# Kernel tuning notes

Measured on AMD Instinct MI355X. Metric: run time of the kernel, lower is better.

## Reference

```python
import jax, jax.numpy as jnp
import numpy as np

N = 100000          # batch_size == number of tree nodes
F = 512             # feature_size
C = 512             # number_of_features_to_detect
WINDOW_DEPTH = 3    # depth_of_sliding_window


def _build_tree(rng, n):
    # random tree: parent[i] < i, node 0 is root (parent[0] = 0)
    parent = np.zeros(n, dtype=np.int32)
    parent[1:] = (rng.random(n - 1) * np.arange(1, n)).astype(np.int32)
    level = np.zeros(n, dtype=np.int32)       # treelib level (root = 0)
    pos = np.zeros(n, dtype=np.int32)         # 0-based index among parent's children
    child_count = np.zeros(n, dtype=np.int32)
    for i in range(1, n):
        p = parent[i]
        level[i] = level[p] + 1
        pos[i] = child_count[p]
        child_count[p] += 1
    sib = child_count[parent] - 1              # treelib siblings() excludes self
    sib[0] = 0                                 # root has no siblings
    pos[0] = 1                                 # special case in get_node_position_amongst_siblings
    return parent, level, pos, sib


def setup_inputs() -> dict:
    key = jax.random.key(0)
    k1, k2, k3, k4, k5 = jax.random.split(key, 5)
    rng = np.random.default_rng(0)
    parent, level, pos, sib = _build_tree(rng, N)
    return {
        "tree_data": jax.random.normal(k1, (N, F), dtype=jnp.float32),
        "W_top": jax.random.normal(k2, (C, F), dtype=jnp.float32),
        "W_left": jax.random.normal(k3, (C, F), dtype=jnp.float32),
        "W_right": jax.random.normal(k4, (C, F), dtype=jnp.float32),
        "bias": jax.random.normal(k5, (C,), dtype=jnp.float32),
        "parent": jnp.asarray(parent),
        "level": jnp.asarray(level),
        "pos": jnp.asarray(pos),
        "sib": jnp.asarray(sib),
    }


def reference(tree_data, W_top, W_left, W_right, bias, parent, level, pos, sib):
    n = tree_data.shape[0]
    f32 = jnp.float32
    # per-node projections with each of the 3 weights: [N, C]
    Yt = tree_data @ W_top.T
    Yl = tree_data @ W_left.T
    Yr = tree_data @ W_right.T
    # edge list: self-edge (window root hovers itself) + child edges
    node_ids = jnp.arange(n, dtype=jnp.int32)
    nodes = jnp.concatenate([node_ids, node_ids[1:]])        # hovered node n_id
    seg = jnp.concatenate([node_ids, parent[1:]])            # window root (output row)
    # coefficients: twc uses the WINDOW ROOT's depth (level+1), rwc/lwc the hovered node
    twc = level[seg].astype(f32) / f32(WINDOW_DEPTH - 1)
    rwc = (1.0 - twc) * ((pos[nodes] - 1).astype(f32)
                         / jnp.maximum(1, sib[nodes] - 1).astype(f32))
    lwc = (1.0 - twc) * (1.0 - rwc)
    contrib = (twc[:, None] * Yt[nodes]
               + lwc[:, None] * Yl[nodes]
               + rwc[:, None] * Yr[nodes]
               + bias)                                        # bias added per hovered node
    summed = jax.ops.segment_sum(contrib, seg, num_segments=n)
    return jnp.tanh(summed)
```

## Files before the change

### kernel.cpp

```cpp
#include <hip/hip_runtime.h>
#include <hip/hip_bf16.h>
#include <stdint.h>

#define F_DIM 512
#define C_DIM 512
#define K3    1536
#define NT    48

typedef _Float16 f16x8 __attribute__((ext_vector_type(8)));
typedef float    f32x4 __attribute__((ext_vector_type(4)));

__device__ __forceinline__ float rho_of(int p, int sb) {
    int d = sb - 1; if (d < 1) d = 1;
    return (float)(p - 1) / (float)d;
}

__device__ __forceinline__ void split2s(float v, _Float16& h, _Float16& m) {
    h = (_Float16)v;
    float r1 = v - (float)h;
    m = (_Float16)(r1 * 2048.0f);
}

__global__ void k_count(const int* __restrict__ parent, int* __restrict__ counts, int n) {
    int c = blockIdx.x * 256 + threadIdx.x;
    if (c >= 1 && c < n) atomicAdd(&counts[parent[c]], 1);
}

__device__ __forceinline__ int blockScanIncl(int v, int* sm) {
    int lane = threadIdx.x & 63;
    int w = threadIdx.x >> 6;
    #pragma unroll
    for (int d = 1; d < 64; d <<= 1) {
        int t = __shfl_up(v, d, 64);
        if (lane >= d) v += t;
    }
    if (lane == 63) sm[w] = v;
    __syncthreads();
    if (threadIdx.x < 64) {
        int s = (threadIdx.x < 16) ? sm[threadIdx.x] : 0;
        #pragma unroll
        for (int d = 1; d < 16; d <<= 1) {
            int t = __shfl_up(s, d, 64);
            if (lane >= d) s += t;
        }
        if (threadIdx.x < 16) sm[threadIdx.x] = s;
    }
    __syncthreads();
    return v + (w > 0 ? sm[w - 1] : 0);
}

__global__ void k_scan1(const int* __restrict__ counts, int* __restrict__ starts,
                        int* __restrict__ bsums, int n) {
    __shared__ int sm[16];
    int i = blockIdx.x * 1024 + threadIdx.x;
    int v = (i < n) ? counts[i] : 0;
    int incl = blockScanIncl(v, sm);
    if (i < n) starts[i] = incl - v;
    if (threadIdx.x == 1023) bsums[blockIdx.x] = incl;
}

__global__ void k_scan2(int* __restrict__ bsums, int nb) {
    __shared__ int sm[16];
    int v = ((int)threadIdx.x < nb) ? bsums[threadIdx.x] : 0;
    int incl = blockScanIncl(v, sm);
    if ((int)threadIdx.x < nb) bsums[threadIdx.x] = incl - v;
}

__global__ void k_scan3(int* __restrict__ starts, const int* __restrict__ bsums, int n) {
    int i = blockIdx.x * 1024 + threadIdx.x;
    if (i < n) starts[i] += bsums[blockIdx.x];
}

__global__ void k_fill(const int* __restrict__ parent, const int* __restrict__ pos,
                       const int* __restrict__ starts, int* __restrict__ childlist, int n) {
    int c = blockIdx.x * 256 + threadIdx.x;
    if (c >= 1 && c < n) childlist[starts[parent[c]] + pos[c]] = c;
}

__global__ void k_bcat(const float* __restrict__ Wt, const float* __restrict__ Wl,
                       const float* __restrict__ Wr,
                       _Float16* __restrict__ Bh, _Float16* __restrict__ Bm) {
    int i = blockIdx.x * 256 + threadIdx.x;
    if (i >= C_DIM * K3) return;
    int j = i / K3, kk = i - j * K3;
    int sec = kk >> 9, f = kk & 511;
    const float* W = (sec == 0) ? Wt : ((sec == 1) ? Wl : Wr);
    float v = W[j * F_DIM + f];
    _Float16 h, m;
    split2s(v, h, m);
    Bh[i] = h; Bm[i] = m;
}

__global__ __launch_bounds__(256)
void k_agg(const float* __restrict__ x, const int* __restrict__ level,
           const int* __restrict__ pos, const int* __restrict__ sib,
           const int* __restrict__ starts, const int* __restrict__ counts,
           const int* __restrict__ childlist,
           _Float16* __restrict__ Ah, _Float16* __restrict__ Am,
           int node0, int cnt) {
    int lane = threadIdx.x & 63;
    int gw = (blockIdx.x * 256 + threadIdx.x) >> 6;
    int nW = (gridDim.x * 256) >> 6;
    for (int i = gw; i < cnt; i += nW) {
        int s = node0 + i;
        float t = 0.5f * (float)level[s];
        float u = 1.0f - t;
        float u2 = u * u;
        float s0[8], s1[8];
        #pragma unroll
        for (int j = 0; j < 8; ++j) { s0[j] = 0.f; s1[j] = 0.f; }
        {
            float r = rho_of(pos[s], sib[s]);
            const float4* xp = (const float4*)(x + (size_t)s * F_DIM) + lane * 2;
            float4 a = xp[0], b = xp[1];
            float vv[8] = {a.x, a.y, a.z, a.w, b.x, b.y, b.z, b.w};
            #pragma unroll
            for (int j = 0; j < 8; ++j) { s0[j] += vv[j]; s1[j] = fmaf(r, vv[j], s1[j]); }
        }
        int cs = starts[s], ne = counts[s];
        for (int e = 0; e < ne; ++e) {
            int c = childlist[cs + e];
            float r = rho_of(pos[c], sib[c]);
            const float4* xp = (const float4*)(x + (size_t)c * F_DIM) + lane * 2;
            float4 a = xp[0], b = xp[1];
            float vv[8] = {a.x, a.y, a.z, a.w, b.x, b.y, b.z, b.w};
            #pragma unroll
            for (int j = 0; j < 8; ++j) { s0[j] += vv[j]; s1[j] = fmaf(r, vv[j], s1[j]); }
        }
        f16x8 ph[3], pm[3];
        #pragma unroll
        for (int j = 0; j < 8; ++j) {
            float a0 = t * s0[j];
            float a1 = fmaf(-u2, s1[j], u * s0[j]);
            float a2 = u * s1[j];
            _Float16 h, m;
            split2s(a0, h, m); ph[0][j] = h; pm[0][j] = m;
            split2s(a1, h, m); ph[1][j] = h; pm[1][j] = m;
            split2s(a2, h, m); ph[2][j] = h; pm[2][j] = m;
        }
        size_t rb = (size_t)i * K3 + (size_t)(lane * 8);
        #pragma unroll
        for (int sec = 0; sec < 3; ++sec) {
            *(f16x8*)(Ah + rb + sec * 512) = ph[sec];
            *(f16x8*)(Am + rb + sec * 512) = pm[sec];
        }
    }
}

__device__ __forceinline__ f32x4 mfma16(f16x8 a, f16x8 b, f32x4 c) {
    return __builtin_amdgcn_mfma_f32_16x16x32_f16(a, b, c, 0, 0, 0);
}

#define AS1 __attribute__((address_space(1)))
#define AS3 __attribute__((address_space(3)))

__global__ __launch_bounds__(256, 2)
void k_gemm(const _Float16* __restrict__ Ah, const _Float16* __restrict__ Am,
            const _Float16* __restrict__ Bh, const _Float16* __restrict__ Bm,
            const float* __restrict__ bias, const int* __restrict__ counts,
            float* __restrict__ out, int Mreal, int row0) {
    __shared__ __align__(16) _Float16 sAh[2][128 * 32];
    __shared__ __align__(16) _Float16 sAm[2][128 * 32];
    __shared__ __align__(16) _Float16 sBh[2][128 * 32];
    __shared__ __align__(16) _Float16 sBm[2][128 * 32];

    int nwg = gridDim.x, bid = blockIdx.x;
    int q = nwg >> 3, r = nwg & 7;
    int xcd = bid & 7, idx = bid >> 3;
    int wg = (xcd < r ? xcd * (q + 1) : r * (q + 1) + (xcd - r) * q) + idx;
    int panel = wg >> 2, colt = wg & 3;
    int m0 = panel * 128, n0 = colt * 128;

    int tid = threadIdx.x;
    int lane = tid & 63, wid = tid >> 6;
    int wm = wid >> 1, wn = wid & 1;
    int l15 = lane & 15, lg = lane >> 4;

    int c0 = tid,        r0 = c0 >> 2, s0g = (c0 & 3) ^ ((r0 >> 1) & 3);
    int c1 = 256 + tid,  r1 = c1 >> 2, s1g = (c1 & 3) ^ ((r1 >> 1) & 3);
    size_t so0 = (size_t)r0 * (K3 * 2) + (size_t)(s0g << 4);
    size_t so1 = (size_t)r1 * (K3 * 2) + (size_t)(s1g << 4);
    const char* gAh0 = (const char*)(Ah + (size_t)m0 * K3) + so0;
    const char* gAh1 = (const char*)(Ah + (size_t)m0 * K3) + so1;
    const char* gAm0 = (const char*)(Am + (size_t)m0 * K3) + so0;
    const char* gAm1 = (const char*)(Am + (size_t)m0 * K3) + so1;
    const char* gBh0 = (const char*)(Bh + (size_t)n0 * K3) + so0;
    const char* gBh1 = (const char*)(Bh + (size_t)n0 * K3) + so1;
    const char* gBm0 = (const char*)(Bm + (size_t)n0 * K3) + so0;
    const char* gBm1 = (const char*)(Bm + (size_t)n0 * K3) + so1;
    int ld0 = (0 * 256 + wid * 64) * 8;
    int ld1 = (1 * 256 + wid * 64) * 8;

    int koff = ((lg ^ ((l15 >> 1) & 3)) << 3);

    f32x4 accH[4][4] = {};
    f32x4 accR[4][4] = {};

#define STAGE(pb, kb)                                                                      \
    do {                                                                                   \
        __builtin_amdgcn_global_load_lds((const AS1 unsigned int*)(gAh0 + (kb)),           \
            (AS3 unsigned int*)(&sAh[pb][ld0]), 16, 0, 0);                                 \
        __builtin_amdgcn_global_load_lds((const AS1 unsigned int*)(gAh1 + (kb)),           \
            (AS3 unsigned int*)(&sAh[pb][ld1]), 16, 0, 0);                                 \
        __builtin_amdgcn_global_load_lds((const AS1 unsigned int*)(gAm0 + (kb)),           \
            (AS3 unsigned int*)(&sAm[pb][ld0]), 16, 0, 0);                                 \
        __builtin_amdgcn_global_load_lds((const AS1 unsigned int*)(gAm1 + (kb)),           \
            (AS3 unsigned int*)(&sAm[pb][ld1]), 16, 0, 0);                                 \
        __builtin_amdgcn_global_load_lds((const AS1 unsigned int*)(gBh0 + (kb)),           \
            (AS3 unsigned int*)(&sBh[pb][ld0]), 16, 0, 0);                                 \
        __builtin_amdgcn_global_load_lds((const AS1 unsigned int*)(gBh1 + (kb)),           \
            (AS3 unsigned int*)(&sBh[pb][ld1]), 16, 0, 0);                                 \
        __builtin_amdgcn_global_load_lds((const AS1 unsigned int*)(gBm0 + (kb)),           \
            (AS3 unsigned int*)(&sBm[pb][ld0]), 16, 0, 0);                                 \
        __builtin_amdgcn_global_load_lds((const AS1 unsigned int*)(gBm1 + (kb)),           \
            (AS3 unsigned int*)(&sBm[pb][ld1]), 16, 0, 0);                                 \
    } while (0)

    STAGE(0, 0);

    for (int t = 0; t < NT; ++t) {
        int p = t & 1;
        if (t + 1 < NT) {
            STAGE(p ^ 1, (size_t)(t + 1) * 64);
            asm volatile("s_waitcnt vmcnt(8)" ::: "memory");
        } else {
            asm volatile("s_waitcnt vmcnt(0)" ::: "memory");
        }
        __builtin_amdgcn_sched_barrier(0);
        __builtin_amdgcn_s_barrier();
        __builtin_amdgcn_sched_barrier(0);

        f16x8 ah[4], am[4], bh[4], bm[4];
        #pragma unroll
        for (int ni = 0; ni < 4; ++ni) {
            int co = (wn * 64 + ni * 16 + l15) * 32 + koff;
            bh[ni] = *(const f16x8*)&sBh[p][co];
            bm[ni] = *(const f16x8*)&sBm[p][co];
        }
        #pragma unroll
        for (int mi = 0; mi < 4; ++mi) {
            int ro = (wm * 64 + mi * 16 + l15) * 32 + koff;
            ah[mi] = *(const f16x8*)&sAh[p][ro];
            am[mi] = *(const f16x8*)&sAm[p][ro];
        }
        asm volatile("s_waitcnt lgkmcnt(0)" ::: "memory");
        __builtin_amdgcn_sched_barrier(0);
        __builtin_amdgcn_s_barrier();
        __builtin_amdgcn_sched_barrier(0);

        __builtin_amdgcn_s_setprio(1);
        #pragma unroll
        for (int mi = 0; mi < 4; ++mi) {
            #pragma unroll
            for (int ni = 0; ni < 4; ++ni) {
                accH[mi][ni] = mfma16(ah[mi], bh[ni], accH[mi][ni]);
                accR[mi][ni] = mfma16(ah[mi], bm[ni], accR[mi][ni]);
                accR[mi][ni] = mfma16(am[mi], bh[ni], accR[mi][ni]);
            }
        }
        __builtin_amdgcn_s_setprio(0);
        __builtin_amdgcn_sched_barrier(0);
    }
#undef STAGE

    const float S1 = 1.0f / 2048.0f;

    #pragma unroll
    for (int mi = 0; mi < 4; ++mi) {
        #pragma unroll
        for (int ni = 0; ni < 4; ++ni) {
            int colL = n0 + wn * 64 + ni * 16 + l15;
            #pragma unroll
            for (int rr = 0; rr < 4; ++rr) {
                int rowL = m0 + wm * 64 + mi * 16 + lg * 4 + rr;
                if (rowL < Mreal) {
                    int g = row0 + rowL;
                    float v = accH[mi][ni][rr]
                              + accR[mi][ni][rr] * S1
                              + (1.0f + (float)counts[g]) * bias[colL];
                    out[(size_t)g * C_DIM + colL] = tanhf(v);
                }
            }
        }
    }
}

extern "C" void kernel_launch(void* const* d_in, const int* in_sizes, int n_in,
                              void* d_out, int out_size, void* d_ws, size_t ws_size,
                              hipStream_t stream) {
    const float* x    = (const float*)d_in[0];
    const float* Wt   = (const float*)d_in[1];
    const float* Wl   = (const float*)d_in[2];
    const float* Wr   = (const float*)d_in[3];
    const float* bias = (const float*)d_in[4];
    const int* parent = (const int*)d_in[5];
    const int* level  = (const int*)d_in[6];
    const int* pos    = (const int*)d_in[7];
    const int* sib    = (const int*)d_in[8];
    const int N = in_sizes[5];
    float* out = (float*)d_out;
    (void)n_in; (void)out_size;

    char* w = (char*)d_ws;
    size_t off = 0;
    auto alloc = [&](size_t bytes) -> void* {
        void* p = w + off;
        off += (bytes + 255) & ~(size_t)255;
        return p;
    };
    int* counts    = (int*)alloc((size_t)N * 4);
    int* starts    = (int*)alloc((size_t)N * 4);
    int* childlist = (int*)alloc((size_t)N * 4);
    int* bsums     = (int*)alloc(1024 * 4);
    _Float16* Bh   = (_Float16*)alloc((size_t)C_DIM * K3 * 2);
    _Float16* Bm   = (_Float16*)alloc((size_t)C_DIM * K3 * 2);

    size_t avail = ws_size > off ? ws_size - off : 0;
    long long Npad = ((long long)N + 127) & ~127LL;
    long long chunkM = (long long)(avail / ((size_t)K3 * 2 * 2)) & ~127LL;
    if (chunkM > Npad) chunkM = Npad;
    if (chunkM < 128) chunkM = 128;
    _Float16* Ah = (_Float16*)alloc((size_t)chunkM * K3 * 2);
    _Float16* Am = (_Float16*)alloc((size_t)chunkM * K3 * 2);

    hipMemsetAsync(counts, 0, (size_t)N * 4, stream);
    int nb256 = (N + 255) / 256;
    int nb1024 = (N + 1023) / 1024;
    k_count<<<nb256, 256, 0, stream>>>(parent, counts, N);
    k_scan1<<<nb1024, 1024, 0, stream>>>(counts, starts, bsums, N);
    k_scan2<<<1, 1024, 0, stream>>>(bsums, nb1024);
    k_scan3<<<nb1024, 1024, 0, stream>>>(starts, bsums, N);
    k_fill<<<nb256, 256, 0, stream>>>(parent, pos, starts, childlist, N);
    k_bcat<<<(C_DIM * K3 + 255) / 256, 256, 0, stream>>>(Wt, Wl, Wr, Bh, Bm);

    for (long long m0 = 0; m0 < N; m0 += chunkM) {
        int mc = (int)((N - m0 < chunkM) ? (N - m0) : chunkM);
        int mcPad = (mc + 127) & ~127;
        k_agg<<<2048, 256, 0, stream>>>(x, level, pos, sib, starts, counts, childlist,
                                        Ah, Am, (int)m0, mc);
        int ntiles = (mcPad / 128) * 4;
        k_gemm<<<ntiles, 256, 0, stream>>>(Ah, Am, Bh, Bm, bias, counts,
                                           out, mc, (int)m0);
    }
}
```

Before: 824.9 us.

## Restructure split-fp16 GEMM into 256x256 tiles with sequential term passes and triple buffering

The GEMM tile grows from 128x128 with 4 waves to 256x256 with 8 waves, each wave owning a 128x64 sub-tile in a single accumulator set. The three split-precision products (Am*Bh, Ah*Bm, then Ah*Bh) now run as sequential K passes, 144 steps in total, instead of three interleaved MFMAs per step. The correction accumulator is scaled by 1/2048 before the high pass starts. Loads use a 3-slot LDS ring issued two steps ahead, with a single barrier per step. This aims to improve operand reuse per byte loaded and overlap loads with MFMAs, at the cost of larger tiles, more padding and fewer workgroups.

```diff
diff --git a/kernel.cpp b/kernel.cpp
--- a/kernel.cpp
+++ b/kernel.cpp
@@ -5,7 +5,8 @@
 #define F_DIM 512
 #define C_DIM 512
 #define K3    1536
-#define NT    48
+#define NTT   144
+#define BKT   32
 
 typedef _Float16 f16x8 __attribute__((ext_vector_type(8)));
 typedef float    f32x4 __attribute__((ext_vector_type(4)));
@@ -154,129 +155,143 @@
 #define AS1 __attribute__((address_space(1)))
 #define AS3 __attribute__((address_space(3)))
 
-__global__ __launch_bounds__(256, 2)
+__global__ __launch_bounds__(512, 2)
 void k_gemm(const _Float16* __restrict__ Ah, const _Float16* __restrict__ Am,
             const _Float16* __restrict__ Bh, const _Float16* __restrict__ Bm,
             const float* __restrict__ bias, const int* __restrict__ counts,
             float* __restrict__ out, int Mreal, int row0) {
-    __shared__ __align__(16) _Float16 sAh[2][128 * 32];
-    __shared__ __align__(16) _Float16 sAm[2][128 * 32];
-    __shared__ __align__(16) _Float16 sBh[2][128 * 32];
-    __shared__ __align__(16) _Float16 sBm[2][128 * 32];
+    __shared__ __align__(16) _Float16 sA[3][256 * 32];
+    __shared__ __align__(16) _Float16 sB[3][256 * 32];
 
     int nwg = gridDim.x, bid = blockIdx.x;
     int q = nwg >> 3, r = nwg & 7;
     int xcd = bid & 7, idx = bid >> 3;
     int wg = (xcd < r ? xcd * (q + 1) : r * (q + 1) + (xcd - r) * q) + idx;
-    int panel = wg >> 2, colt = wg & 3;
-    int m0 = panel * 128, n0 = colt * 128;
+    int panel = wg >> 1, colt = wg & 1;
+    int m0 = panel * 256, n0 = colt * 256;
 
     int tid = threadIdx.x;
     int lane = tid & 63, wid = tid >> 6;
-    int wm = wid >> 1, wn = wid & 1;
+    int wm = wid >> 2, wn = wid & 3;
     int l15 = lane & 15, lg = lane >> 4;
 
-    int c0 = tid,        r0 = c0 >> 2, s0g = (c0 & 3) ^ ((r0 >> 1) & 3);
-    int c1 = 256 + tid,  r1 = c1 >> 2, s1g = (c1 & 3) ^ ((r1 >> 1) & 3);
-    size_t so0 = (size_t)r0 * (K3 * 2) + (size_t)(s0g << 4);
-    size_t so1 = (size_t)r1 * (K3 * 2) + (size_t)(s1g << 4);
-    const char* gAh0 = (const char*)(Ah + (size_t)m0 * K3) + so0;
-    const char* gAh1 = (const char*)(Ah + (size_t)m0 * K3) + so1;
-    const char* gAm0 = (const char*)(Am + (size_t)m0 * K3) + so0;
-    const char* gAm1 = (const char*)(Am + (size_t)m0 * K3) + so1;
-    const char* gBh0 = (const char*)(Bh + (size_t)n0 * K3) + so0;
-    const char* gBh1 = (const char*)(Bh + (size_t)n0 * K3) + so1;
-    const char* gBm0 = (const char*)(Bm + (size_t)n0 * K3) + so0;
-    const char* gBm1 = (const char*)(Bm + (size_t)n0 * K3) + so1;
-    int ld0 = (0 * 256 + wid * 64) * 8;
-    int ld1 = (1 * 256 + wid * 64) * 8;
-
-    int koff = ((lg ^ ((l15 >> 1) & 3)) << 3);
-
-    f32x4 accH[4][4] = {};
-    f32x4 accR[4][4] = {};
-
-#define STAGE(pb, kb)                                                                      \
+    const char* gAh = (const char*)(Ah + (size_t)m0 * K3);
+    const char* gAm = (const char*)(Am + (size_t)m0 * K3);
+    const char* gBh = (const char*)(Bh + (size_t)n0 * K3);
+    const char* gBm = (const char*)(Bm + (size_t)n0 * K3);
+
+    int ch0 = tid, ch1 = 512 + tid;
+    int r0 = ch0 >> 2, s0 = (ch0 & 3) ^ ((r0 >> 1) & 3);
+    int r1 = ch1 >> 2, s1 = (ch1 & 3) ^ ((r1 >> 1) & 3);
+    int go0 = r0 * (K3 * 2) + (s0 << 4);
+    int go1 = r1 * (K3 * 2) + (s1 << 4);
+    int ldo0 = (0 * 512 + wid * 64) * 8;
+    int ldo1 = (1 * 512 + wid * 64) * 8;
+
+    int kswz = (lg ^ ((l15 >> 1) & 3)) << 3;
+
+    f32x4 acc[8][4] = {};
+
+#define ISSUE_A(tt)                                                                        \
     do {                                                                                   \
-        __builtin_amdgcn_global_load_lds((const AS1 unsigned int*)(gAh0 + (kb)),           \
-            (AS3 unsigned int*)(&sAh[pb][ld0]), 16, 0, 0);                                 \
-        __builtin_amdgcn_global_load_lds((const AS1 unsigned int*)(gAh1 + (kb)),           \
-            (AS3 unsigned int*)(&sAh[pb][ld1]), 16, 0, 0);                                 \
-        __builtin_amdgcn_global_load_lds((const AS1 unsigned int*)(gAm0 + (kb)),           \
-            (AS3 unsigned int*)(&sAm[pb][ld0]), 16, 0, 0);                                 \
-        __builtin_amdgcn_global_load_lds((const AS1 unsigned int*)(gAm1 + (kb)),           \
-            (AS3 unsigned int*)(&sAm[pb][ld1]), 16, 0, 0);                                 \
-        __builtin_amdgcn_global_load_lds((const AS1 unsigned int*)(gBh0 + (kb)),           \
-            (AS3 unsigned int*)(&sBh[pb][ld0]), 16, 0, 0);                                 \
-        __builtin_amdgcn_global_load_lds((const AS1 unsigned int*)(gBh1 + (kb)),           \
-            (AS3 unsigned int*)(&sBh[pb][ld1]), 16, 0, 0);                                 \
-        __builtin_amdgcn_global_load_lds((const AS1 unsigned int*)(gBm0 + (kb)),           \
-            (AS3 unsigned int*)(&sBm[pb][ld0]), 16, 0, 0);                                 \
-        __builtin_amdgcn_global_load_lds((const AS1 unsigned int*)(gBm1 + (kb)),           \
-            (AS3 unsigned int*)(&sBm[pb][ld1]), 16, 0, 0);                                 \
+        int sg_ = (tt) >= 96 ? 2 : ((tt) >= 48 ? 1 : 0);                                   \
+        int kb_ = ((tt) - sg_ * 48) * (BKT * 2);                                           \
+        const char* ab_ = (sg_ == 0) ? gAm : gAh;                                          \
+        int sl_ = (tt) % 3;                                                                \
+        __builtin_amdgcn_global_load_lds((const AS1 unsigned int*)(ab_ + go0 + kb_),       \
+            (AS3 unsigned int*)(&sA[sl_][ldo0]), 16, 0, 0);                                \
+        __builtin_amdgcn_global_load_lds((const AS1 unsigned int*)(ab_ + go1 + kb_),       \
+            (AS3 unsigned int*)(&sA[sl_][ldo1]), 16, 0, 0);                                \
     } while (0)
-
-    STAGE(0, 0);
-
-    for (int t = 0; t < NT; ++t) {
-        int p = t & 1;
-        if (t + 1 < NT) {
-            STAGE(p ^ 1, (size_t)(t + 1) * 64);
-            asm volatile("s_waitcnt vmcnt(8)" ::: "memory");
-        } else {
+#define ISSUE_B(tt)                                                                        \
+    do {                                                                                   \
+        int sg_ = (tt) >= 96 ? 2 : ((tt) >= 48 ? 1 : 0);                                   \
+        int kb_ = ((tt) - sg_ * 48) * (BKT * 2);                                           \
+        const char* bb_ = (sg_ == 1) ? gBm : gBh;                                          \
+        int sl_ = (tt) % 3;                                                                \
+        __builtin_amdgcn_global_load_lds((const AS1 unsigned int*)(bb_ + go0 + kb_),       \
+            (AS3 unsigned int*)(&sB[sl_][ldo0]), 16, 0, 0);                                \
+        __builtin_amdgcn_global_load_lds((const AS1 unsigned int*)(bb_ + go1 + kb_),       \
+            (AS3 unsigned int*)(&sB[sl_][ldo1]), 16, 0, 0);                                \
+    } while (0)
+
+    ISSUE_A(0); ISSUE_B(0);
+    ISSUE_A(1); ISSUE_B(1);
+    ISSUE_A(2); ISSUE_B(2);
+    asm volatile("s_waitcnt vmcnt(8)" ::: "memory");
+    __builtin_amdgcn_sched_barrier(0);
+    __builtin_amdgcn_s_barrier();
+    __builtin_amdgcn_sched_barrier(0);
+
+    for (int T = 0; T < NTT; ++T) {
+        int sl = T % 3;
+        const _Float16* pA = sA[sl];
+        const _Float16* pB = sB[sl];
+
+        if (T == 96) {
+            #pragma unroll
+            for (int mi = 0; mi < 8; ++mi)
+                #pragma unroll
+                for (int ni = 0; ni < 4; ++ni)
+                    acc[mi][ni] *= (1.0f / 2048.0f);
+        }
+
+        f16x8 bf[4], af[4];
+        #pragma unroll
+        for (int ni = 0; ni < 4; ++ni) {
+            int ro = wn * 64 + ni * 16 + l15;
+            bf[ni] = *(const f16x8*)&pB[ro * 32 + kswz];
+        }
+        #pragma unroll
+        for (int mi = 0; mi < 4; ++mi) {
+            int ro = wm * 128 + mi * 16 + l15;
+            af[mi] = *(const f16x8*)&pA[ro * 32 + kswz];
+        }
+        if (T + 2 < NTT) ISSUE_A(T + 2);
+        __builtin_amdgcn_s_setprio(1);
+        #pragma unroll
+        for (int mi = 0; mi < 4; ++mi)
+            #pragma unroll
+            for (int ni = 0; ni < 4; ++ni)
+                acc[mi][ni] = mfma16(af[mi], bf[ni], acc[mi][ni]);
+        __builtin_amdgcn_s_setprio(0);
+
+        #pragma unroll
+        for (int mi = 0; mi < 4; ++mi) {
+            int ro = wm * 128 + (mi + 4) * 16 + l15;
+            af[mi] = *(const f16x8*)&pA[ro * 32 + kswz];
+        }
+        if (T + 2 < NTT) ISSUE_B(T + 2);
+        __builtin_amdgcn_s_setprio(1);
+        #pragma unroll
+        for (int mi = 0; mi < 4; ++mi)
+            #pragma unroll
+            for (int ni = 0; ni < 4; ++ni)
+                acc[mi + 4][ni] = mfma16(af[mi], bf[ni], acc[mi + 4][ni]);
+        __builtin_amdgcn_s_setprio(0);
+
+        if (T < NTT - 2)
+            asm volatile("s_waitcnt vmcnt(4)" ::: "memory");
+        else
             asm volatile("s_waitcnt vmcnt(0)" ::: "memory");
-        }
         __builtin_amdgcn_sched_barrier(0);
         __builtin_amdgcn_s_barrier();
         __builtin_amdgcn_sched_barrier(0);
-
-        f16x8 ah[4], am[4], bh[4], bm[4];
-        #pragma unroll
-        for (int ni = 0; ni < 4; ++ni) {
-            int co = (wn * 64 + ni * 16 + l15) * 32 + koff;
-            bh[ni] = *(const f16x8*)&sBh[p][co];
-            bm[ni] = *(const f16x8*)&sBm[p][co];
-        }
-        #pragma unroll
-        for (int mi = 0; mi < 4; ++mi) {
-            int ro = (wm * 64 + mi * 16 + l15) * 32 + koff;
-            ah[mi] = *(const f16x8*)&sAh[p][ro];
-            am[mi] = *(const f16x8*)&sAm[p][ro];
-        }
-        asm volatile("s_waitcnt lgkmcnt(0)" ::: "memory");
-        __builtin_amdgcn_sched_barrier(0);
-        __builtin_amdgcn_s_barrier();
-        __builtin_amdgcn_sched_barrier(0);
-
-        __builtin_amdgcn_s_setprio(1);
-        #pragma unroll
-        for (int mi = 0; mi < 4; ++mi) {
-            #pragma unroll
-            for (int ni = 0; ni < 4; ++ni) {
-                accH[mi][ni] = mfma16(ah[mi], bh[ni], accH[mi][ni]);
-                accR[mi][ni] = mfma16(ah[mi], bm[ni], accR[mi][ni]);
-                accR[mi][ni] = mfma16(am[mi], bh[ni], accR[mi][ni]);
-            }
-        }
-        __builtin_amdgcn_s_setprio(0);
-        __builtin_amdgcn_sched_barrier(0);
-    }
-#undef STAGE
-
-    const float S1 = 1.0f / 2048.0f;
+    }
+#undef ISSUE_A
+#undef ISSUE_B
 
     #pragma unroll
-    for (int mi = 0; mi < 4; ++mi) {
+    for (int mi = 0; mi < 8; ++mi) {
         #pragma unroll
         for (int ni = 0; ni < 4; ++ni) {
             int colL = n0 + wn * 64 + ni * 16 + l15;
             #pragma unroll
             for (int rr = 0; rr < 4; ++rr) {
-                int rowL = m0 + wm * 64 + mi * 16 + lg * 4 + rr;
+                int rowL = m0 + wm * 128 + mi * 16 + lg * 4 + rr;
                 if (rowL < Mreal) {
                     int g = row0 + rowL;
-                    float v = accH[mi][ni][rr]
-                              + accR[mi][ni][rr] * S1
+                    float v = acc[mi][ni][rr]
                               + (1.0f + (float)counts[g]) * bias[colL];
                     out[(size_t)g * C_DIM + colL] = tanhf(v);
                 }
@@ -316,10 +331,10 @@
     _Float16* Bm   = (_Float16*)alloc((size_t)C_DIM * K3 * 2);
 
     size_t avail = ws_size > off ? ws_size - off : 0;
-    long long Npad = ((long long)N + 127) & ~127LL;
-    long long chunkM = (long long)(avail / ((size_t)K3 * 2 * 2)) & ~127LL;
+    long long Npad = ((long long)N + 255) & ~255LL;
+    long long chunkM = (long long)(avail / ((size_t)K3 * 2 * 2)) & ~255LL;
     if (chunkM > Npad) chunkM = Npad;
-    if (chunkM < 128) chunkM = 128;
+    if (chunkM < 256) chunkM = 256;
     _Float16* Ah = (_Float16*)alloc((size_t)chunkM * K3 * 2);
     _Float16* Am = (_Float16*)alloc((size_t)chunkM * K3 * 2);
 
@@ -335,11 +350,11 @@
 
     for (long long m0 = 0; m0 < N; m0 += chunkM) {
         int mc = (int)((N - m0 < chunkM) ? (N - m0) : chunkM);
-        int mcPad = (mc + 127) & ~127;
+        int mcPad = (mc + 255) & ~255;
         k_agg<<<2048, 256, 0, stream>>>(x, level, pos, sib, starts, counts, childlist,
                                         Ah, Am, (int)m0, mc);
-        int ntiles = (mcPad / 128) * 4;
-        k_gemm<<<ntiles, 256, 0, stream>>>(Ah, Am, Bh, Bm, bias, counts,
+        int ntiles = (mcPad / 256) * 2;
+        k_gemm<<<ntiles, 512, 0, stream>>>(Ah, Am, Bh, Bm, bias, counts,
                                            out, mc, (int)m0);
     }
 }
```

Result: slower. 913.1 us (+10.7%).
